# Kernel tuning notes

Hardware: AMD Instinct MI355X
Metric: run time of the kernel (lower is better)

The kernel has to match this reference:

```python
import jax, jax.numpy as jnp
import numpy as np

B, N = 64, 2048
CON, FUSE, HID = 512, 1024, 512

def setup_inputs() -> dict:
    key = jax.random.key(0)
    k1, k2, k3, k4, k5, k6 = jax.random.split(key, 6)
    confounder_set = jax.random.normal(k1, (B, N, CON), dtype=jnp.float32)
    fuse_rep = jax.random.normal(k2, (B, FUSE), dtype=jnp.float32)
    probabilities = jax.random.uniform(k3, (B, N, 1), dtype=jnp.float32)
    # Linear weights, torch nn.Linear style: y = x @ W.T, init ~ U(-1/sqrt(in), 1/sqrt(in))
    Wq = jax.random.uniform(k4, (HID, FUSE), minval=-1.0, maxval=1.0, dtype=jnp.float32) / np.sqrt(FUSE)
    Wk = jax.random.uniform(k5, (HID, CON), minval=-1.0, maxval=1.0, dtype=jnp.float32) / np.sqrt(CON)
    Wt = jax.random.uniform(k6, (1, HID), minval=-1.0, maxval=1.0, dtype=jnp.float32) / np.sqrt(HID)
    return {"confounder_set": confounder_set, "fuse_rep": fuse_rep,
            "probabilities": probabilities, "Wq": Wq, "Wk": Wk, "Wt": Wt}

def reference(confounder_set, fuse_rep, probabilities, Wq, Wk, Wt):
    # query: [B, H]; key: [B, N, H]
    query = jnp.einsum('bf,hf->bh', fuse_rep, Wq)
    k = jnp.einsum('bnc,hc->bnh', confounder_set, Wk)
    fuse = jnp.tanh(query[:, None, :] + k)          # [B, N, H]
    scores = jnp.einsum('bnh,oh->bno', fuse, Wt)    # [B, N, 1]
    attn = jax.nn.softmax(scores, axis=1)           # softmax over set dim
    fin = jnp.sum(attn * confounder_set * probabilities, axis=1)  # [B, CON]
    return fin
```

## Files before the change

### kernel.cpp

```cpp
#include <hip/hip_runtime.h>
#include <hip/hip_bf16.h>
#include <stdint.h>

#define BB   64
#define NN   2048
#define CONC 512
#define FUSEF 1024
#define HIDH 512

typedef short  bf16x8 __attribute__((ext_vector_type(8)));
typedef unsigned short u16x8 __attribute__((ext_vector_type(8)));
typedef float  f32x4  __attribute__((ext_vector_type(4)));

#define GLOBAL_U32(p) ((const __attribute__((address_space(1))) unsigned int*)(p))
#define LDS_U32(p)    ((__attribute__((address_space(3))) unsigned int*)(p))

__device__ __forceinline__ unsigned short f2bf(float f) {
    unsigned u = __builtin_bit_cast(unsigned, f);
    u += 0x7fffu + ((u >> 16) & 1u);
    return (unsigned short)(u >> 16);
}

__device__ __forceinline__ float fast_tanh(float x) {
    return 1.0f - 2.0f / (__expf(2.0f * x) + 1.0f);
}

__global__ __launch_bounds__(512)
void query_kernel(const float* __restrict__ fuse, const float* __restrict__ wq,
                  float* __restrict__ query) {
    __shared__ float fs[FUSEF];
    const int b = blockIdx.x, tid = threadIdx.x;
    fs[tid]       = fuse[b * FUSEF + tid];
    fs[tid + 512] = fuse[b * FUSEF + tid + 512];
    __syncthreads();
    const float* w = wq + (long)tid * FUSEF;
    float a0 = 0.f, a1 = 0.f, a2 = 0.f, a3 = 0.f;
    #pragma unroll 4
    for (int f = 0; f < FUSEF; f += 4) {
        float4 wf = *(const float4*)(w + f);
        a0 += wf.x * fs[f];     a1 += wf.y * fs[f + 1];
        a2 += wf.z * fs[f + 2]; a3 += wf.w * fs[f + 3];
    }
    query[b * HIDH + tid] = (a0 + a1) + (a2 + a3);
}

__global__ __launch_bounds__(256)
void pack_wk(const float* __restrict__ wk, char* __restrict__ wkb) {
    const int u  = blockIdx.x * 256 + threadIdx.x;
    const int h  = u >> 6;
    const int k0 = (u & 63) << 3;
    const float* src = wk + (long)h * CONC + k0;
    float4 f0 = *(const float4*)src;
    float4 f1 = *(const float4*)(src + 4);
    u16x8 v;
    v[0] = f2bf(f0.x); v[1] = f2bf(f0.y); v[2] = f2bf(f0.z); v[3] = f2bf(f0.w);
    v[4] = f2bf(f1.x); v[5] = f2bf(f1.y); v[6] = f2bf(f1.z); v[7] = f2bf(f1.w);
    const int kk = k0 >> 6, kloc = k0 & 63;
    const int off = kk * 65536 + h * 128 + (((kloc * 2)) ^ ((h & 7) << 4));
    *(u16x8*)(wkb + off) = v;
}

__global__ __launch_bounds__(512)
void score_kernel(const float* __restrict__ conf, const char* __restrict__ wkb,
                  const float* __restrict__ query, const float* __restrict__ wt,
                  float* __restrict__ scores) {
    __shared__ __align__(16) char As[64 * 128];
    __shared__ __align__(16) char Bs[512 * 128];
    __shared__ float qs[HIDH];
    __shared__ float wts[HIDH];
    __shared__ float sp[64];

    const int tid  = threadIdx.x;
    const int lane = tid & 63;
    const int wid  = tid >> 6;
    const int wr   = wid >> 2;
    const int wc   = wid & 3;
    const long row0 = (long)blockIdx.x * 64;
    const int  b    = (int)(row0 >> 11);

    qs[tid]  = query[b * HIDH + tid];
    wts[tid] = wt[tid];
    if (tid < 64) sp[tid] = 0.f;

    f32x4 acc[2][8] = {};

    const float* aGlob = conf + row0 * CONC;
    const int arow = tid >> 3;
    const int akc  = (tid & 7) << 3;
    const int aoff = arow * 128 + (((akc * 2)) ^ ((arow & 7) << 4));

    for (int kk = 0; kk < 8; ++kk) {
        {
            const float* src = aGlob + (long)arow * CONC + kk * 64 + akc;
            float4 f0 = *(const float4*)src;
            float4 f1 = *(const float4*)(src + 4);
            u16x8 v;
            v[0] = f2bf(f0.x); v[1] = f2bf(f0.y); v[2] = f2bf(f0.z); v[3] = f2bf(f0.w);
            v[4] = f2bf(f1.x); v[5] = f2bf(f1.y); v[6] = f2bf(f1.z); v[7] = f2bf(f1.w);
            *(u16x8*)(As + aoff) = v;
        }
        {
            const char* btile = wkb + kk * 65536;
            #pragma unroll
            for (int i = 0; i < 8; ++i) {
                const int off = wid * 8192 + i * 1024;
                __builtin_amdgcn_global_load_lds(
                    GLOBAL_U32(btile + off + (lane << 4)),
                    LDS_U32(Bs + off),
                    16, 0, 0);
            }
        }
        __syncthreads();
        #pragma unroll
        for (int ks = 0; ks < 2; ++ks) {
            const int kb = (ks * 32 + ((lane >> 4) << 3)) * 2;
            bf16x8 af[2];
            #pragma unroll
            for (int rf = 0; rf < 2; ++rf) {
                const int r = wr * 32 + rf * 16 + (lane & 15);
                af[rf] = *(const bf16x8*)(As + r * 128 + (kb ^ ((r & 7) << 4)));
            }
            bf16x8 bfr[8];
            #pragma unroll
            for (int cf = 0; cf < 8; ++cf) {
                const int h = wc * 128 + cf * 16 + (lane & 15);
                bfr[cf] = *(const bf16x8*)(Bs + h * 128 + (kb ^ ((h & 7) << 4)));
            }
            #pragma unroll
            for (int rf = 0; rf < 2; ++rf)
                #pragma unroll
                for (int cf = 0; cf < 8; ++cf)
                    acc[rf][cf] = __builtin_amdgcn_mfma_f32_16x16x32_bf16(
                        af[rf], bfr[cf], acc[rf][cf], 0, 0, 0);
        }
        __syncthreads();
    }

    float ps[2][4] = {};
    const int cb = wc * 128 + (lane & 15);
    #pragma unroll
    for (int rf = 0; rf < 2; ++rf)
        #pragma unroll
        for (int cf = 0; cf < 8; ++cf) {
            const int col = cb + cf * 16;
            const float q = qs[col], w = wts[col];
            #pragma unroll
            for (int j = 0; j < 4; ++j)
                ps[rf][j] += fast_tanh(acc[rf][cf][j] + q) * w;
        }
    #pragma unroll
    for (int m = 1; m < 16; m <<= 1) {
        #pragma unroll
        for (int rf = 0; rf < 2; ++rf)
            #pragma unroll
            for (int j = 0; j < 4; ++j)
                ps[rf][j] += __shfl_xor(ps[rf][j], m);
    }
    if ((lane & 15) == 0) {
        const int rb = wr * 32 + ((lane >> 4) << 2);
        #pragma unroll
        for (int rf = 0; rf < 2; ++rf)
            #pragma unroll
            for (int j = 0; j < 4; ++j)
                atomicAdd(&sp[rb + rf * 16 + j], ps[rf][j]);
    }
    __syncthreads();
    if (tid < 64) scores[row0 + tid] = sp[tid];
}

__global__ __launch_bounds__(256)
void out_kernel(const float* __restrict__ conf, const float* __restrict__ prob,
                const float* __restrict__ scores, float* __restrict__ fin) {
    __shared__ float wl[NN];
    __shared__ float4 red[16 * 16];
    __shared__ float smax[4], ssum[4];

    const int tid = threadIdx.x;
    const int b   = blockIdx.x >> 3;
    const int c0  = (blockIdx.x & 7) * 64;
    const float* sc = scores + b * NN;

    float mx = -1e30f;
    for (int n = tid; n < NN; n += 256) mx = fmaxf(mx, sc[n]);
    #pragma unroll
    for (int m = 1; m < 64; m <<= 1) mx = fmaxf(mx, __shfl_xor(mx, m));
    if ((tid & 63) == 0) smax[tid >> 6] = mx;
    __syncthreads();
    mx = fmaxf(fmaxf(smax[0], smax[1]), fmaxf(smax[2], smax[3]));

    float sm = 0.f;
    const float* pb = prob + b * NN;
    for (int n = tid; n < NN; n += 256) {
        const float e = __expf(sc[n] - mx);
        wl[n] = e * pb[n];
        sm += e;
    }
    #pragma unroll
    for (int m = 1; m < 64; m <<= 1) sm += __shfl_xor(sm, m);
    if ((tid & 63) == 0) ssum[tid >> 6] = sm;
    __syncthreads();
    const float rsum = 1.0f / (ssum[0] + ssum[1] + ssum[2] + ssum[3]);

    const int c4 = (tid & 15) << 2;
    const int ng = tid >> 4;
    const float* cb = conf + (long)b * NN * CONC + c0 + c4;
    float4 acc = make_float4(0.f, 0.f, 0.f, 0.f);
    for (int n = ng; n < NN; n += 16) {
        const float w = wl[n];
        float4 v = *(const float4*)(cb + (long)n * CONC);
        acc.x += w * v.x; acc.y += w * v.y; acc.z += w * v.z; acc.w += w * v.w;
    }
    red[ng * 16 + (tid & 15)] = acc;
    __syncthreads();
    if (tid < 16) {
        float4 s = red[tid];
        #pragma unroll
        for (int g = 1; g < 16; ++g) {
            float4 t = red[g * 16 + tid];
            s.x += t.x; s.y += t.y; s.z += t.z; s.w += t.w;
        }
        s.x *= rsum; s.y *= rsum; s.z *= rsum; s.w *= rsum;
        *(float4*)(fin + b * CONC + c0 + (tid << 2)) = s;
    }
}

extern "C" void kernel_launch(void* const* d_in, const int* in_sizes, int n_in,
                              void* d_out, int out_size, void* d_ws, size_t ws_size,
                              hipStream_t stream) {
    const float* conf = (const float*)d_in[0];
    const float* fuse = (const float*)d_in[1];
    const float* prob = (const float*)d_in[2];
    const float* wq   = (const float*)d_in[3];
    const float* wk   = (const float*)d_in[4];
    const float* wt   = (const float*)d_in[5];
    float* out = (float*)d_out;
    char* ws = (char*)d_ws;

    float* q_ws  = (float*)ws;
    float* sc_ws = (float*)(ws + 131072);
    char*  wkb   = ws + 655360;

    query_kernel<<<dim3(BB), dim3(512), 0, stream>>>(fuse, wq, q_ws);
    pack_wk<<<dim3(128), dim3(256), 0, stream>>>(wk, wkb);
    score_kernel<<<dim3((BB * NN) / 64), dim3(512), 0, stream>>>(conf, wkb, q_ws, wt, sc_ws);
    out_kernel<<<dim3(BB * 8), dim3(256), 0, stream>>>(conf, prob, sc_ws, out);
}
```

Baseline: 545.8 us.

## Split hidden dim across score blocks and split set dim in output reduction

The score kernel now splits the 512-wide hidden dimension into two halves on a second grid axis. Each block holds half the Wk tile in LDS and keeps half the accumulators, which is meant to raise occupancy. The cost is that every confounder tile is loaded and converted twice. The output kernel now splits the set dimension into 16 chunks per batch and writes partial sums that a new reduce kernel adds up, and the query kernel spreads its work over more blocks. Together these aim for more parallelism and fewer registers and less LDS per block, at the price of redundant A loads and an extra launch.

Result: faster. 512.2 us (-6.2%).

```diff
diff --git a/kernel.cpp b/kernel.cpp
--- a/kernel.cpp
+++ b/kernel.cpp
@@ -25,23 +25,34 @@
     return 1.0f - 2.0f / (__expf(2.0f * x) + 1.0f);
 }
 
-__global__ __launch_bounds__(512)
+__global__ __launch_bounds__(256)
 void query_kernel(const float* __restrict__ fuse, const float* __restrict__ wq,
                   float* __restrict__ query) {
-    __shared__ float fs[FUSEF];
-    const int b = blockIdx.x, tid = threadIdx.x;
-    fs[tid]       = fuse[b * FUSEF + tid];
-    fs[tid + 512] = fuse[b * FUSEF + tid + 512];
-    __syncthreads();
-    const float* w = wq + (long)tid * FUSEF;
+    __shared__ float fsh[FUSEF];
+    const int tid = threadIdx.x;
+    const int b   = blockIdx.x >> 3;
+    const int hcq = blockIdx.x & 7;
+    fsh[tid]       = fuse[b * FUSEF + tid];
+    fsh[tid + 256] = fuse[b * FUSEF + tid + 256];
+    fsh[tid + 512] = fuse[b * FUSEF + tid + 512];
+    fsh[tid + 768] = fuse[b * FUSEF + tid + 768];
+    __syncthreads();
+    const int hl = tid >> 2;
+    const int fs = tid & 3;
+    const int h  = hcq * 64 + hl;
+    const float* w  = wq + (long)h * FUSEF + fs * 256;
+    const float* fl = fsh + fs * 256;
     float a0 = 0.f, a1 = 0.f, a2 = 0.f, a3 = 0.f;
-    #pragma unroll 4
-    for (int f = 0; f < FUSEF; f += 4) {
-        float4 wf = *(const float4*)(w + f);
-        a0 += wf.x * fs[f];     a1 += wf.y * fs[f + 1];
-        a2 += wf.z * fs[f + 2]; a3 += wf.w * fs[f + 3];
-    }
-    query[b * HIDH + tid] = (a0 + a1) + (a2 + a3);
+    #pragma unroll 8
+    for (int i = 0; i < 256; i += 4) {
+        float4 wf = *(const float4*)(w + i);
+        a0 += wf.x * fl[i];     a1 += wf.y * fl[i + 1];
+        a2 += wf.z * fl[i + 2]; a3 += wf.w * fl[i + 3];
+    }
+    float s = (a0 + a1) + (a2 + a3);
+    s += __shfl_xor(s, 1);
+    s += __shfl_xor(s, 2);
+    if (fs == 0) query[b * HIDH + h] = s;
 }
 
 __global__ __launch_bounds__(256)
@@ -55,39 +66,34 @@
     u16x8 v;
     v[0] = f2bf(f0.x); v[1] = f2bf(f0.y); v[2] = f2bf(f0.z); v[3] = f2bf(f0.w);
     v[4] = f2bf(f1.x); v[5] = f2bf(f1.y); v[6] = f2bf(f1.z); v[7] = f2bf(f1.w);
-    const int kk = k0 >> 6, kloc = k0 & 63;
-    const int off = kk * 65536 + h * 128 + (((kloc * 2)) ^ ((h & 7) << 4));
+    const int hc = h >> 8, hl = h & 255, kk = k0 >> 6, kloc = k0 & 63;
+    const int off = hc * 262144 + kk * 32768 + hl * 128 + (((kloc * 2)) ^ ((hl & 7) << 4));
     *(u16x8*)(wkb + off) = v;
 }
 
-__global__ __launch_bounds__(512)
+__global__ __launch_bounds__(512, 6)
 void score_kernel(const float* __restrict__ conf, const char* __restrict__ wkb,
                   const float* __restrict__ query, const float* __restrict__ wt,
-                  float* __restrict__ scores) {
+                  float* __restrict__ sc_part) {
     __shared__ __align__(16) char As[64 * 128];
-    __shared__ __align__(16) char Bs[512 * 128];
-    __shared__ float qs[HIDH];
-    __shared__ float wts[HIDH];
-    __shared__ float sp[64];
+    __shared__ __align__(16) char Bs[256 * 128];
 
     const int tid  = threadIdx.x;
     const int lane = tid & 63;
     const int wid  = tid >> 6;
     const int wr   = wid >> 2;
     const int wc   = wid & 3;
-    const long row0 = (long)blockIdx.x * 64;
+    const int hc   = blockIdx.x;
+    const long row0 = (long)blockIdx.y * 64;
     const int  b    = (int)(row0 >> 11);
 
-    qs[tid]  = query[b * HIDH + tid];
-    wts[tid] = wt[tid];
-    if (tid < 64) sp[tid] = 0.f;
-
-    f32x4 acc[2][8] = {};
+    f32x4 acc[2][4] = {};
 
     const float* aGlob = conf + row0 * CONC;
     const int arow = tid >> 3;
     const int akc  = (tid & 7) << 3;
     const int aoff = arow * 128 + (((akc * 2)) ^ ((arow & 7) << 4));
+    const char* bbase = wkb + hc * 262144;
 
     for (int kk = 0; kk < 8; ++kk) {
         {
@@ -100,14 +106,12 @@
             *(u16x8*)(As + aoff) = v;
         }
         {
-            const char* btile = wkb + kk * 65536;
-            #pragma unroll
-            for (int i = 0; i < 8; ++i) {
-                const int off = wid * 8192 + i * 1024;
-                __builtin_amdgcn_global_load_lds(
-                    GLOBAL_U32(btile + off + (lane << 4)),
-                    LDS_U32(Bs + off),
-                    16, 0, 0);
+            const char* btile = bbase + kk * 32768;
+            #pragma unroll
+            for (int i = 0; i < 4; ++i) {
+                const int off = wid * 4096 + i * 1024;
+                __builtin_amdgcn_global_load_lds(GLOBAL_U32(btile + off + (lane << 4)),
+                                                 LDS_U32(Bs + off), 16, 0, 0);
             }
         }
         __syncthreads();
@@ -120,68 +124,77 @@
                 const int r = wr * 32 + rf * 16 + (lane & 15);
                 af[rf] = *(const bf16x8*)(As + r * 128 + (kb ^ ((r & 7) << 4)));
             }
-            bf16x8 bfr[8];
-            #pragma unroll
-            for (int cf = 0; cf < 8; ++cf) {
-                const int h = wc * 128 + cf * 16 + (lane & 15);
-                bfr[cf] = *(const bf16x8*)(Bs + h * 128 + (kb ^ ((h & 7) << 4)));
+            bf16x8 bfr[4];
+            #pragma unroll
+            for (int cf = 0; cf < 4; ++cf) {
+                const int hl2 = wc * 64 + cf * 16 + (lane & 15);
+                bfr[cf] = *(const bf16x8*)(Bs + hl2 * 128 + (kb ^ ((hl2 & 7) << 4)));
             }
             #pragma unroll
             for (int rf = 0; rf < 2; ++rf)
                 #pragma unroll
-                for (int cf = 0; cf < 8; ++cf)
+                for (int cf = 0; cf < 4; ++cf)
                     acc[rf][cf] = __builtin_amdgcn_mfma_f32_16x16x32_bf16(
                         af[rf], bfr[cf], acc[rf][cf], 0, 0, 0);
         }
         __syncthreads();
     }
 
+    float* spf = (float*)As;
+    float qv[4], wv[4];
+    #pragma unroll
+    for (int cf = 0; cf < 4; ++cf) {
+        const int c = wc * 64 + cf * 16 + (lane & 15);
+        qv[cf] = query[b * HIDH + hc * 256 + c];
+        wv[cf] = wt[hc * 256 + c];
+    }
     float ps[2][4] = {};
-    const int cb = wc * 128 + (lane & 15);
     #pragma unroll
     for (int rf = 0; rf < 2; ++rf)
         #pragma unroll
-        for (int cf = 0; cf < 8; ++cf) {
-            const int col = cb + cf * 16;
-            const float q = qs[col], w = wts[col];
+        for (int cf = 0; cf < 4; ++cf)
             #pragma unroll
             for (int j = 0; j < 4; ++j)
-                ps[rf][j] += fast_tanh(acc[rf][cf][j] + q) * w;
-        }
-    #pragma unroll
-    for (int m = 1; m < 16; m <<= 1) {
+                ps[rf][j] += fast_tanh(acc[rf][cf][j] + qv[cf]) * wv[cf];
+
+    if (tid < 64) spf[tid] = 0.f;
+    __syncthreads();
+    #pragma unroll
+    for (int m = 1; m < 16; m <<= 1)
         #pragma unroll
         for (int rf = 0; rf < 2; ++rf)
             #pragma unroll
             for (int j = 0; j < 4; ++j)
                 ps[rf][j] += __shfl_xor(ps[rf][j], m);
-    }
     if ((lane & 15) == 0) {
         const int rb = wr * 32 + ((lane >> 4) << 2);
         #pragma unroll
         for (int rf = 0; rf < 2; ++rf)
             #pragma unroll
             for (int j = 0; j < 4; ++j)
-                atomicAdd(&sp[rb + rf * 16 + j], ps[rf][j]);
-    }
-    __syncthreads();
-    if (tid < 64) scores[row0 + tid] = sp[tid];
+                atomicAdd(&spf[rb + rf * 16 + j], ps[rf][j]);
+    }
+    __syncthreads();
+    if (tid < 64) sc_part[(long)hc * (BB * NN) + row0 + tid] = spf[tid];
 }
 
 __global__ __launch_bounds__(256)
 void out_kernel(const float* __restrict__ conf, const float* __restrict__ prob,
-                const float* __restrict__ scores, float* __restrict__ fin) {
-    __shared__ float wl[NN];
-    __shared__ float4 red[16 * 16];
+                const float* __restrict__ sc0, const float* __restrict__ sc1,
+                float* __restrict__ part) {
+    __shared__ float wl[128];
+    __shared__ float4 red4[128];
     __shared__ float smax[4], ssum[4];
 
     const int tid = threadIdx.x;
-    const int b   = blockIdx.x >> 3;
-    const int c0  = (blockIdx.x & 7) * 64;
-    const float* sc = scores + b * NN;
+    const int b   = blockIdx.x >> 4;
+    const int ns  = blockIdx.x & 15;
+    const int n0  = ns * 128;
+    const float* s0 = sc0 + b * NN;
+    const float* s1 = sc1 + b * NN;
 
     float mx = -1e30f;
-    for (int n = tid; n < NN; n += 256) mx = fmaxf(mx, sc[n]);
+    for (int n = tid; n < NN; n += 256) mx = fmaxf(mx, s0[n] + s1[n]);
     #pragma unroll
     for (int m = 1; m < 64; m <<= 1) mx = fmaxf(mx, __shfl_xor(mx, m));
     if ((tid & 63) == 0) smax[tid >> 6] = mx;
@@ -189,39 +202,46 @@
     mx = fmaxf(fmaxf(smax[0], smax[1]), fmaxf(smax[2], smax[3]));
 
     float sm = 0.f;
-    const float* pb = prob + b * NN;
-    for (int n = tid; n < NN; n += 256) {
-        const float e = __expf(sc[n] - mx);
-        wl[n] = e * pb[n];
-        sm += e;
-    }
+    for (int n = tid; n < NN; n += 256) sm += __expf(s0[n] + s1[n] - mx);
     #pragma unroll
     for (int m = 1; m < 64; m <<= 1) sm += __shfl_xor(sm, m);
     if ((tid & 63) == 0) ssum[tid >> 6] = sm;
     __syncthreads();
     const float rsum = 1.0f / (ssum[0] + ssum[1] + ssum[2] + ssum[3]);
 
-    const int c4 = (tid & 15) << 2;
-    const int ng = tid >> 4;
-    const float* cb = conf + (long)b * NN * CONC + c0 + c4;
+    if (tid < 128) {
+        const int n = n0 + tid;
+        wl[tid] = __expf(s0[n] + s1[n] - mx) * prob[b * NN + n];
+    }
+    __syncthreads();
+
+    const int tcol = tid & 127;
+    const int trow = tid >> 7;
+    const int col4 = tcol << 2;
+    const float* cbase = conf + ((long)b * NN + n0) * CONC + col4;
     float4 acc = make_float4(0.f, 0.f, 0.f, 0.f);
-    for (int n = ng; n < NN; n += 16) {
-        const float w = wl[n];
-        float4 v = *(const float4*)(cb + (long)n * CONC);
+    for (int r = trow; r < 128; r += 2) {
+        const float w = wl[r];
+        float4 v = *(const float4*)(cbase + (long)r * CONC);
         acc.x += w * v.x; acc.y += w * v.y; acc.z += w * v.z; acc.w += w * v.w;
     }
-    red[ng * 16 + (tid & 15)] = acc;
-    __syncthreads();
-    if (tid < 16) {
-        float4 s = red[tid];
-        #pragma unroll
-        for (int g = 1; g < 16; ++g) {
-            float4 t = red[g * 16 + tid];
-            s.x += t.x; s.y += t.y; s.z += t.z; s.w += t.w;
-        }
-        s.x *= rsum; s.y *= rsum; s.z *= rsum; s.w *= rsum;
-        *(float4*)(fin + b * CONC + c0 + (tid << 2)) = s;
-    }
+    if (trow == 1) red4[tcol] = acc;
+    __syncthreads();
+    if (trow == 0) {
+        float4 t = red4[tcol];
+        acc.x = (acc.x + t.x) * rsum; acc.y = (acc.y + t.y) * rsum;
+        acc.z = (acc.z + t.z) * rsum; acc.w = (acc.w + t.w) * rsum;
+        *(float4*)(part + ((long)ns * BB + b) * CONC + col4) = acc;
+    }
+}
+
+__global__ __launch_bounds__(256)
+void reduce_kernel(const float* __restrict__ part, float* __restrict__ fin) {
+    const int idx = blockIdx.x * 256 + threadIdx.x;
+    float s = 0.f;
+    #pragma unroll
+    for (int ns = 0; ns < 16; ++ns) s += part[ns * (BB * CONC) + idx];
+    fin[idx] = s;
 }
 
 extern "C" void kernel_launch(void* const* d_in, const int* in_sizes, int n_in,
@@ -238,10 +258,12 @@
 
     float* q_ws  = (float*)ws;
     float* sc_ws = (float*)(ws + 131072);
-    char*  wkb   = ws + 655360;
-
-    query_kernel<<<dim3(BB), dim3(512), 0, stream>>>(fuse, wq, q_ws);
+    char*  wkb   = ws + 131072 + 1048576;
+    float* part  = (float*)(ws + 131072 + 1048576 + 524288);
+
+    query_kernel<<<dim3(BB * 8), dim3(256), 0, stream>>>(fuse, wq, q_ws);
     pack_wk<<<dim3(128), dim3(256), 0, stream>>>(wk, wkb);
-    score_kernel<<<dim3((BB * NN) / 64), dim3(512), 0, stream>>>(conf, wkb, q_ws, wt, sc_ws);
-    out_kernel<<<dim3(BB * 8), dim3(256), 0, stream>>>(conf, prob, sc_ws, out);
-}
+    score_kernel<<<dim3(2, 2048), dim3(512), 0, stream>>>(conf, wkb, q_ws, wt, sc_ws);
+    out_kernel<<<dim3(BB * 16), dim3(256), 0, stream>>>(conf, prob, sc_ws, sc_ws + BB * NN, part);
+    reduce_kernel<<<dim3(128), dim3(256), 0, stream>>>(part, out);
+}
```
